# Kernel optimization log

Hardware: AMD Instinct MI355X
Metric: run time of the kernel (lower is better)

Reference implementation:

```python
import jax, jax.numpy as jnp
import numpy as np

D_MODEL = 1024
N_HEADS = 16
D_K = D_MODEL // N_HEADS
SCALE = float(np.sqrt(D_K))


def setup_inputs() -> dict:
    key = jax.random.key(0)
    ks = jax.random.split(key, 6)
    B, S = 2, 2048
    lim_qkv = 1.0 / np.sqrt(D_MODEL)
    x = jax.random.normal(ks[0], (B, S, D_MODEL), dtype=jnp.float32)
    mask = jnp.ones((B, S), dtype=jnp.int32)
    W_qkv = jax.random.uniform(ks[1], (D_MODEL, 3 * D_MODEL), jnp.float32, -lim_qkv, lim_qkv)
    b_qkv = jax.random.uniform(ks[2], (3 * D_MODEL,), jnp.float32, -lim_qkv, lim_qkv)
    W_out = jax.random.uniform(ks[3], (D_MODEL, D_MODEL), jnp.float32, -lim_qkv, lim_qkv)
    b_out = jax.random.uniform(ks[4], (D_MODEL,), jnp.float32, -lim_qkv, lim_qkv)
    return {"x": x, "mask": mask, "W_qkv": W_qkv, "b_qkv": b_qkv, "W_out": W_out, "b_out": b_out}


def reference(x, mask, W_qkv, b_qkv, W_out, b_out):
    B, S, _ = x.shape
    qkv = x @ W_qkv + b_qkv                                  # [B,S,3*D]
    qkv = qkv.reshape(B, S, 3, N_HEADS, D_K)
    qkv = jnp.transpose(qkv, (2, 0, 3, 1, 4))                # [3,B,H,S,Dk]
    q, k, v = qkv[0], qkv[1], qkv[2]
    scores = jnp.einsum('bhqd,bhkd->bhqk', q, k) / SCALE      # [B,H,S,S]
    m = mask[:, None, None, :]                               # [B,1,1,S]
    scores = jnp.where(m == 0, jnp.float32(-1e9), scores)
    attn = jax.nn.softmax(scores, axis=-1)
    out = jnp.einsum('bhqk,bhkd->bhqd', attn, v)             # [B,H,S,Dk]
    out = jnp.transpose(out, (0, 2, 1, 3)).reshape(B, S, D_MODEL)
    return out @ W_out + b_out
```

## Files before the change

kernel.cpp:

```cpp
#include <hip/hip_runtime.h>
#include <hip/hip_bf16.h>

typedef __attribute__((ext_vector_type(8))) short short8;
typedef __attribute__((ext_vector_type(4))) short short4v;
typedef __attribute__((ext_vector_type(4))) float f32x4;
typedef __attribute__((ext_vector_type(16))) float f32x16;
typedef __attribute__((ext_vector_type(4))) unsigned uint4v;
typedef __attribute__((ext_vector_type(2))) unsigned uint2v;

static constexpr int BATCH = 2, S = 2048, D = 1024, H = 16, DK = 64;
static constexpr int TOK = BATCH * S;
static constexpr int NQKV = 3 * D;
static constexpr float C2 = 0.125f * 1.44269504088896f;

__device__ inline unsigned short f2bf(float f) {
  unsigned int u = __builtin_bit_cast(unsigned int, f);
  unsigned int r = (u + 0x7fffu + ((u >> 16) & 1u)) >> 16;
  return (unsigned short)r;
}

__device__ inline unsigned cvt_pk_bf16(float lo, float hi) {
  unsigned r;
  asm("v_cvt_pk_bf16_f32 %0, %1, %2" : "=v"(r) : "v"(lo), "v"(hi));
  return r;
}

__device__ inline uint2v permswap(unsigned a, unsigned b) {
  return __builtin_amdgcn_permlane32_swap(a, b, false, false);
}

__device__ inline float fexp2(float x) { return __builtin_amdgcn_exp2f(x); }

__device__ inline void gload_lds16(const void* g, void* l) {
  __builtin_amdgcn_global_load_lds((const __attribute__((address_space(1))) void*)g,
                                   (__attribute__((address_space(3))) void*)l, 16, 0, 0);
}

static constexpr int NB_CVT  = (TOK * D / 4) / 256;
static constexpr int NB_WQKV = (NQKV / 32) * (D / 32);
static constexpr int NB_WOUT = (D / 32) * (D / 32);
static constexpr int NB_MASK = TOK / 256;

__global__ __launch_bounds__(256) void k_prep(const float* __restrict__ x,
                                              unsigned short* __restrict__ x_bf,
                                              const float* __restrict__ W_qkv,
                                              unsigned short* __restrict__ wqkv_t,
                                              const float* __restrict__ W_out,
                                              unsigned short* __restrict__ wout_t,
                                              const int* __restrict__ mask,
                                              float* __restrict__ maskadd,
                                              unsigned char* __restrict__ tileflags) {
  __shared__ float tile[32][33];
  const int bi = blockIdx.x;
  const int tid = threadIdx.x;
  if (bi < NB_CVT) {
    const int i = bi * 256 + tid;
    const float4 v = ((const float4*)x)[i];
    short4v o;
    o[0] = (short)f2bf(v.x); o[1] = (short)f2bf(v.y);
    o[2] = (short)f2bf(v.z); o[3] = (short)f2bf(v.w);
    ((short4v*)x_bf)[i] = o;
    return;
  }
  if (bi < NB_CVT + NB_WQKV + NB_WOUT) {
    const int tbi = bi - NB_CVT;
    const float* in; unsigned short* out; int C, bx, by;
    if (tbi < NB_WQKV) { in = W_qkv; out = wqkv_t; C = NQKV; bx = tbi % (NQKV / 32); by = tbi / (NQKV / 32); }
    else { const int u = tbi - NB_WQKV; in = W_out; out = wout_t; C = D; bx = u % (D / 32); by = u / (D / 32); }
    const int tx = tid & 31, ty = tid >> 5;
    const int bc = bx * 32, br = by * 32;
#pragma unroll
    for (int i = 0; i < 32; i += 8)
      tile[ty + i][tx] = in[(size_t)(br + ty + i) * C + bc + tx];
    __syncthreads();
#pragma unroll
    for (int i = 0; i < 32; i += 8)
      out[(size_t)(bc + ty + i) * D + br + tx] = f2bf(tile[tx][ty + i]);
    return;
  }
  {
    const int j = (bi - NB_CVT - NB_WQKV - NB_WOUT) * 256 + tid;
    const int mv = mask[j];
    maskadd[j] = mv ? 0.f : -1.0e9f;
    const unsigned long long bal = __ballot(mv == 0);
    if ((tid & 63) == 0) tileflags[j >> 6] = (bal != 0ull) ? 1 : 0;
  }
}

template <int QKV_MODE>
__global__ __launch_bounds__(256, 3) void k_gemm(const unsigned short* __restrict__ A,
                                                 const unsigned short* __restrict__ Bt,
                                                 const float* __restrict__ bias,
                                                 void* __restrict__ Cout,
                                                 unsigned short* __restrict__ vt,
                                                 int M, int N, int K) {
  __shared__ alignas(16) unsigned short As[128 * 64];
  __shared__ alignas(16) unsigned short Bs[128 * 64];
  const int tid = threadIdx.x;
  const int wid = tid >> 6, lane = tid & 63;
  const int lr = lane & 15, lg = lane >> 4;
  const int nbx = N >> 7;
  const int bx = blockIdx.x % nbx, by = blockIdx.x / nbx;
  const int m0 = by << 7, n0 = bx << 7;
  const int wm = (wid >> 1) << 6, wn = (wid & 1) << 6;

  f32x4 acc[4][4] = {};

  const int sk = ((lane & 7) ^ (lane >> 3)) << 4;
  const int srow = lane >> 3;

  const int ktc = K >> 6;
  for (int kt = 0; kt < ktc; ++kt) {
    const int k0 = kt << 6;
    __syncthreads();
#pragma unroll
    for (int c = 0; c < 4; ++c) {
      const int chunk = c * 4 + wid;
      const int mrow = chunk * 8 + srow;
      const char* ga = (const char*)(A + (size_t)(m0 + mrow) * K + k0) + sk;
      gload_lds16(ga, (char*)As + chunk * 1024);
      const char* gb = (const char*)(Bt + (size_t)(n0 + mrow) * K + k0) + sk;
      gload_lds16(gb, (char*)Bs + chunk * 1024);
    }
    __syncthreads();
#pragma unroll
    for (int ks = 0; ks < 2; ++ks) {
      const int kb = ks * 64 + lg * 16;
      const int swz = (lr & 7) << 4;
      short8 af[4], bfr[4];
#pragma unroll
      for (int mf = 0; mf < 4; ++mf) {
        const int m = wm + mf * 16 + lr;
        af[mf] = *(const short8*)((const char*)As + m * 128 + (kb ^ swz));
      }
#pragma unroll
      for (int nf = 0; nf < 4; ++nf) {
        const int n = wn + nf * 16 + lr;
        bfr[nf] = *(const short8*)((const char*)Bs + n * 128 + (kb ^ swz));
      }
#pragma unroll
      for (int mf = 0; mf < 4; ++mf)
#pragma unroll
        for (int nf = 0; nf < 4; ++nf)
          acc[mf][nf] = __builtin_amdgcn_mfma_f32_16x16x32_bf16(af[mf], bfr[nf], acc[mf][nf], 0, 0, 0);
    }
  }
#pragma unroll
  for (int nf = 0; nf < 4; ++nf) {
    const int n = n0 + wn + nf * 16 + lr;
    const float bv = bias[n];
    if (QKV_MODE) {
      if (n < 2 * D) {
        const float scl = (n < D) ? C2 : 1.0f;
#pragma unroll
        for (int mf = 0; mf < 4; ++mf)
#pragma unroll
          for (int r = 0; r < 4; ++r) {
            const int m = m0 + wm + mf * 16 + lg * 4 + r;
            ((unsigned short*)Cout)[(size_t)m * N + n] = f2bf((acc[mf][nf][r] + bv) * scl);
          }
      } else {
        const int dd = n - 2 * D;
        const int hh = dd >> 6, dk = dd & 63;
#pragma unroll
        for (int mf = 0; mf < 4; ++mf) {
          const int mbase = m0 + wm + mf * 16 + lg * 4;
          const int bb = mbase >> 11;
          const int ss = mbase & (S - 1);
          uint2 w;
          w.x = cvt_pk_bf16(acc[mf][nf][0] + bv, acc[mf][nf][1] + bv);
          w.y = cvt_pk_bf16(acc[mf][nf][2] + bv, acc[mf][nf][3] + bv);
          *(uint2*)(vt + ((size_t)((bb * H + hh) * DK + dk)) * S + ss) = w;
        }
      }
    } else {
#pragma unroll
      for (int mf = 0; mf < 4; ++mf)
#pragma unroll
        for (int r = 0; r < 4; ++r) {
          const int m = m0 + wm + mf * 16 + lg * 4 + r;
          ((float*)Cout)[(size_t)m * N + n] = acc[mf][nf][r] + bv;
        }
    }
  }
}

__global__ __launch_bounds__(256, 2) void k_attn(const unsigned short* __restrict__ qkv,
                                                 const unsigned short* __restrict__ vt,
                                                 const float* __restrict__ maskadd,
                                                 const unsigned char* __restrict__ tileflags,
                                                 unsigned short* __restrict__ attn) {
  __shared__ alignas(16) char Ks[2][16384];
  __shared__ alignas(16) char Vs[2][16384];

  constexpr int NT = S / 128;

  const int blk = blockIdx.x;
  const int work = (blk & 7) * 64 + (blk >> 3);
  const int qt = work & 15;
  const int bh = work >> 4;
  const int b = bh >> 4, h = bh & 15;
  const int tid = threadIdx.x;
  const int wid = tid >> 6, lane = tid & 63;
  const int l5 = lane & 31, hw = lane >> 5;
  const int q0 = qt * 128 + wid * 32;
  const int q = q0 + l5;

  const unsigned char* bflags = tileflags + b * (S / 64);

  const unsigned short* qrow = qkv + (size_t)(b * S + q) * NQKV + h * DK;
  short8 qf[4];
#pragma unroll
  for (int ks = 0; ks < 4; ++ks)
    qf[ks] = *(const short8*)(qrow + ks * 16 + hw * 8);

  const unsigned short* kg0 = qkv + ((size_t)b * S * NQKV + D + h * DK);
  const unsigned short* vg0 = vt + (size_t)bh * DK * S;
  const int srow8 = lane >> 3;
  const int skk = ((lane & 7) ^ srow8) << 4;
  const int vrow4 = lane >> 4;

  auto stage = [&](int buf, int kt) {
    const int kbase = kt * 128;
#pragma unroll
    for (int i = 0; i < 4; ++i) {
      const int ck = wid + i * 4;
      const int krow = ck * 8 + srow8;
      gload_lds16((const char*)(kg0 + (size_t)(kbase + krow) * NQKV) + skk,
                  Ks[buf] + ck * 1024);
      const int cv = wid + i * 4;
      const int vr = cv * 4 + vrow4;
      const int ss = (lane & 15) ^ (vr & 15);
      gload_lds16((const char*)(vg0 + (size_t)vr * S + kbase + ss * 8),
                  Vs[buf] + cv * 1024);
    }
  };

  f32x16 o[2] = {};
  float lpart = 0.f;

  const int rswz8 = (l5 & 7) << 4;
  const int rswz16 = (l5 & 15) << 4;

  stage(0, 0);

  int cur = 0;
  for (int kt = 0; kt < NT; ++kt) {
    asm volatile("s_waitcnt vmcnt(0)" ::: "memory");
    __builtin_amdgcn_s_barrier();
    __builtin_amdgcn_sched_barrier(0);
    if (kt + 1 < NT) stage(cur ^ 1, kt + 1);

    const int kbase = kt * 128;

    f32x16 sc[4];
    __builtin_amdgcn_s_setprio(1);
#pragma unroll
    for (int kh = 0; kh < 4; ++kh) {
      f32x16 t2 = {};
#pragma unroll
      for (int ks = 0; ks < 4; ++ks) {
        const short8 kf = *(const short8*)(Ks[cur] + (kh * 32 + l5) * 128 +
                                           ((ks * 32 + hw * 16) ^ rswz8));
        t2 = __builtin_amdgcn_mfma_f32_32x32x16_bf16(kf, qf[ks], t2, 0, 0, 0);
      }
      sc[kh] = t2;
    }
    __builtin_amdgcn_s_setprio(0);

    short8 vf[2][8];
#pragma unroll
    for (int dh = 0; dh < 2; ++dh)
#pragma unroll
      for (int s = 0; s < 8; ++s)
        vf[dh][s] = *(const short8*)(Vs[cur] + (dh * 32 + l5) * 256 +
                                     ((s * 32 + hw * 16) ^ rswz16));

    if (bflags[2 * kt] | bflags[2 * kt + 1]) {
#pragma unroll
      for (int kh = 0; kh < 4; ++kh)
#pragma unroll
        for (int m = 0; m < 4; ++m) {
          const f32x4 a4 = *(const f32x4*)(maskadd + b * S + kbase + kh * 32 + m * 8 + hw * 4);
#pragma unroll
          for (int r = 0; r < 4; ++r)
            sc[kh][m * 4 + r] += a4[r];
        }
    }

    float ps = 0.f;
#pragma unroll
    for (int kh = 0; kh < 4; ++kh) {
#pragma unroll
      for (int r = 0; r < 16; ++r)
        sc[kh][r] = fexp2(sc[kh][r]);
#pragma unroll
      for (int m = 0; m < 4; ++m)
        ps += (sc[kh][4 * m] + sc[kh][4 * m + 1]) + (sc[kh][4 * m + 2] + sc[kh][4 * m + 3]);

      const unsigned c00 = cvt_pk_bf16(sc[kh][0], sc[kh][1]);
      const unsigned c01 = cvt_pk_bf16(sc[kh][2], sc[kh][3]);
      const unsigned c10 = cvt_pk_bf16(sc[kh][4], sc[kh][5]);
      const unsigned c11 = cvt_pk_bf16(sc[kh][6], sc[kh][7]);
      const unsigned c20 = cvt_pk_bf16(sc[kh][8], sc[kh][9]);
      const unsigned c21 = cvt_pk_bf16(sc[kh][10], sc[kh][11]);
      const unsigned c30 = cvt_pk_bf16(sc[kh][12], sc[kh][13]);
      const unsigned c31 = cvt_pk_bf16(sc[kh][14], sc[kh][15]);
      const uint2v r0 = permswap(c00, c10);
      const uint2v r1 = permswap(c01, c11);
      const uint2v r2 = permswap(c20, c30);
      const uint2v r3 = permswap(c21, c31);
      uint4v p0, p1;
      p0[0] = r0[0]; p0[2] = r0[1]; p0[1] = r1[0]; p0[3] = r1[1];
      p1[0] = r2[0]; p1[2] = r2[1]; p1[1] = r3[0]; p1[3] = r3[1];
      const short8 pb0 = __builtin_bit_cast(short8, p0);
      const short8 pb1 = __builtin_bit_cast(short8, p1);

      __builtin_amdgcn_s_setprio(1);
#pragma unroll
      for (int dh = 0; dh < 2; ++dh) {
        o[dh] = __builtin_amdgcn_mfma_f32_32x32x16_bf16(vf[dh][2 * kh], pb0, o[dh], 0, 0, 0);
        o[dh] = __builtin_amdgcn_mfma_f32_32x32x16_bf16(vf[dh][2 * kh + 1], pb1, o[dh], 0, 0, 0);
      }
      __builtin_amdgcn_s_setprio(0);
    }
    lpart += ps;

    cur ^= 1;
  }

  const float ls = lpart + __shfl_xor(lpart, 32);
  const float inv = 1.0f / ls;
  unsigned short* orow = attn + (size_t)(b * S + q) * D + h * DK;
#pragma unroll
  for (int dh = 0; dh < 2; ++dh)
#pragma unroll
    for (int m = 0; m < 4; ++m) {
      const int d = dh * 32 + m * 8 + hw * 4;
      uint2 w;
      w.x = cvt_pk_bf16(o[dh][4 * m + 0] * inv, o[dh][4 * m + 1] * inv);
      w.y = cvt_pk_bf16(o[dh][4 * m + 2] * inv, o[dh][4 * m + 3] * inv);
      *(uint2*)(orow + d) = w;
    }
}

extern "C" void kernel_launch(void* const* d_in, const int* in_sizes, int n_in,
                              void* d_out, int out_size, void* d_ws, size_t ws_size,
                              hipStream_t stream) {
  const float* x = (const float*)d_in[0];
  const int* mask = (const int*)d_in[1];
  const float* W_qkv = (const float*)d_in[2];
  const float* b_qkv = (const float*)d_in[3];
  const float* W_out = (const float*)d_in[4];
  const float* b_out = (const float*)d_in[5];
  float* out = (float*)d_out;

  char* ws = (char*)d_ws;
  unsigned short* x_bf   = (unsigned short*)(ws);
  unsigned short* wqkv_t = (unsigned short*)(ws + (size_t)(8 << 20));
  unsigned short* wout_t = (unsigned short*)(ws + (size_t)(14 << 20));
  unsigned short* qkv    = (unsigned short*)(ws + (size_t)(16 << 20));
  unsigned short* vtr    = (unsigned short*)(ws + (size_t)(40 << 20));
  unsigned short* attn   = (unsigned short*)(ws + (size_t)(48 << 20));
  float*          madd   = (float*)(ws + (size_t)(56 << 20));
  unsigned char*  tflags = (unsigned char*)(ws + (size_t)(56 << 20) + 16384);

  k_prep<<<NB_CVT + NB_WQKV + NB_WOUT + NB_MASK, 256, 0, stream>>>(
      x, x_bf, W_qkv, wqkv_t, W_out, wout_t, mask, madd, tflags);
  k_gemm<1><<<(TOK / 128) * (NQKV / 128), 256, 0, stream>>>(x_bf, wqkv_t, b_qkv, qkv, vtr, TOK, NQKV, D);
  k_attn<<<BATCH * H * (S / 128), 256, 0, stream>>>(qkv, vtr, madd, tflags, attn);
  k_gemm<0><<<(TOK / 128) * (D / 128), 256, 0, stream>>>(attn, wout_t, b_out, out, nullptr, TOK, D, D);
}
```

Measured before the change: 105.6 us.

## Split attention key range into two halves with a separate combine kernel

```diff
diff --git a/kernel.cpp b/kernel.cpp
--- a/kernel.cpp
+++ b/kernel.cpp
@@ -11,12 +11,17 @@
 static constexpr int BATCH = 2, S = 2048, D = 1024, H = 16, DK = 64;
 static constexpr int TOK = BATCH * S;
 static constexpr int NQKV = 3 * D;
+static constexpr int NBH = BATCH * H;
 static constexpr float C2 = 0.125f * 1.44269504088896f;
 
 __device__ inline unsigned short f2bf(float f) {
   unsigned int u = __builtin_bit_cast(unsigned int, f);
   unsigned int r = (u + 0x7fffu + ((u >> 16) & 1u)) >> 16;
   return (unsigned short)r;
+}
+
+__device__ inline float bf2f(unsigned short u) {
+  return __builtin_bit_cast(float, (unsigned)u << 16);
 }
 
 __device__ inline unsigned cvt_pk_bf16(float lo, float hi) {
@@ -185,26 +190,31 @@
   }
 }
 
-__global__ __launch_bounds__(256, 2) void k_attn(const unsigned short* __restrict__ qkv,
+__global__ __launch_bounds__(512, 4) void k_attn(const unsigned short* __restrict__ qkv,
                                                  const unsigned short* __restrict__ vt,
                                                  const float* __restrict__ maskadd,
                                                  const unsigned char* __restrict__ tileflags,
-                                                 unsigned short* __restrict__ attn) {
+                                                 unsigned short* __restrict__ po0,
+                                                 unsigned short* __restrict__ po1,
+                                                 float* __restrict__ lbuf) {
   __shared__ alignas(16) char Ks[2][16384];
   __shared__ alignas(16) char Vs[2][16384];
 
-  constexpr int NT = S / 128;
+  constexpr int NTH = 8;
 
   const int blk = blockIdx.x;
   const int work = (blk & 7) * 64 + (blk >> 3);
-  const int qt = work & 15;
   const int bh = work >> 4;
+  const int rem = work & 15;
+  const int qt = rem >> 1;
+  const int half = rem & 1;
   const int b = bh >> 4, h = bh & 15;
   const int tid = threadIdx.x;
   const int wid = tid >> 6, lane = tid & 63;
   const int l5 = lane & 31, hw = lane >> 5;
-  const int q0 = qt * 128 + wid * 32;
+  const int q0 = qt * 256 + wid * 32;
   const int q = q0 + l5;
+  const int kt0 = half * NTH;
 
   const unsigned char* bflags = tileflags + b * (S / 64);
 
@@ -223,12 +233,12 @@
   auto stage = [&](int buf, int kt) {
     const int kbase = kt * 128;
 #pragma unroll
-    for (int i = 0; i < 4; ++i) {
-      const int ck = wid + i * 4;
+    for (int i = 0; i < 2; ++i) {
+      const int ck = wid + i * 8;
       const int krow = ck * 8 + srow8;
       gload_lds16((const char*)(kg0 + (size_t)(kbase + krow) * NQKV) + skk,
                   Ks[buf] + ck * 1024);
-      const int cv = wid + i * 4;
+      const int cv = wid + i * 8;
       const int vr = cv * 4 + vrow4;
       const int ss = (lane & 15) ^ (vr & 15);
       gload_lds16((const char*)(vg0 + (size_t)vr * S + kbase + ss * 8),
@@ -242,14 +252,15 @@
   const int rswz8 = (l5 & 7) << 4;
   const int rswz16 = (l5 & 15) << 4;
 
-  stage(0, 0);
+  stage(0, kt0);
 
   int cur = 0;
-  for (int kt = 0; kt < NT; ++kt) {
+  for (int t = 0; t < NTH; ++t) {
+    const int kt = kt0 + t;
     asm volatile("s_waitcnt vmcnt(0)" ::: "memory");
     __builtin_amdgcn_s_barrier();
     __builtin_amdgcn_sched_barrier(0);
-    if (kt + 1 < NT) stage(cur ^ 1, kt + 1);
+    if (t + 1 < NTH) stage(cur ^ 1, kt + 1);
 
     const int kbase = kt * 128;
 
@@ -330,18 +341,48 @@
   }
 
   const float ls = lpart + __shfl_xor(lpart, 32);
-  const float inv = 1.0f / ls;
+  unsigned short* po = (half ? po1 : po0) + ((size_t)bh * S + q) * DK;
+#pragma unroll
+  for (int dh = 0; dh < 2; ++dh)
+#pragma unroll
+    for (int m = 0; m < 4; ++m) {
+      uint2 w;
+      w.x = cvt_pk_bf16(o[dh][4 * m + 0], o[dh][4 * m + 1]);
+      w.y = cvt_pk_bf16(o[dh][4 * m + 2], o[dh][4 * m + 3]);
+      *(uint2*)(po + dh * 32 + m * 8 + hw * 4) = w;
+    }
+  if (hw == 0) lbuf[((size_t)(half * NBH + bh)) * S + q] = ls;
+}
+
+__global__ __launch_bounds__(256) void k_combine(const unsigned short* __restrict__ po0,
+                                                 const unsigned short* __restrict__ po1,
+                                                 const float* __restrict__ lbuf,
+                                                 unsigned short* __restrict__ attn) {
+  const int bh = blockIdx.x >> 3;
+  const int q = ((blockIdx.x & 7) << 8) + threadIdx.x;
+  const int b = bh >> 4, h = bh & 15;
+
+  const float l0 = lbuf[(size_t)bh * S + q];
+  const float l1 = lbuf[((size_t)(NBH + bh)) * S + q];
+  const float inv = 1.0f / (l0 + l1);
+
+  const unsigned short* r0 = po0 + ((size_t)bh * S + q) * DK;
+  const unsigned short* r1 = po1 + ((size_t)bh * S + q) * DK;
   unsigned short* orow = attn + (size_t)(b * S + q) * D + h * DK;
 #pragma unroll
-  for (int dh = 0; dh < 2; ++dh)
-#pragma unroll
-    for (int m = 0; m < 4; ++m) {
-      const int d = dh * 32 + m * 8 + hw * 4;
-      uint2 w;
-      w.x = cvt_pk_bf16(o[dh][4 * m + 0] * inv, o[dh][4 * m + 1] * inv);
-      w.y = cvt_pk_bf16(o[dh][4 * m + 2] * inv, o[dh][4 * m + 3] * inv);
-      *(uint2*)(orow + d) = w;
-    }
+  for (int c = 0; c < 8; ++c) {
+    const short8 a = *(const short8*)(r0 + c * 8);
+    const short8 bb = *(const short8*)(r1 + c * 8);
+    unsigned wv[4];
+#pragma unroll
+    for (int p = 0; p < 4; ++p) {
+      const float v0 = (bf2f((unsigned short)a[2 * p]) + bf2f((unsigned short)bb[2 * p])) * inv;
+      const float v1 = (bf2f((unsigned short)a[2 * p + 1]) + bf2f((unsigned short)bb[2 * p + 1])) * inv;
+      wv[p] = cvt_pk_bf16(v0, v1);
+    }
+    uint4v u; u[0] = wv[0]; u[1] = wv[1]; u[2] = wv[2]; u[3] = wv[3];
+    *(uint4v*)(orow + c * 8) = u;
+  }
 }
 
 extern "C" void kernel_launch(void* const* d_in, const int* in_sizes, int n_in,
@@ -361,13 +402,17 @@
   unsigned short* wout_t = (unsigned short*)(ws + (size_t)(14 << 20));
   unsigned short* qkv    = (unsigned short*)(ws + (size_t)(16 << 20));
   unsigned short* vtr    = (unsigned short*)(ws + (size_t)(40 << 20));
-  unsigned short* attn   = (unsigned short*)(ws + (size_t)(48 << 20));
   float*          madd   = (float*)(ws + (size_t)(56 << 20));
   unsigned char*  tflags = (unsigned char*)(ws + (size_t)(56 << 20) + 16384);
+  float*          lbuf   = (float*)(ws + (size_t)(56 << 20) + 65536);
+  unsigned short* po0    = x_bf;
+  unsigned short* po1    = (unsigned short*)(ws + (size_t)(48 << 20));
+  unsigned short* attn   = qkv;
 
   k_prep<<<NB_CVT + NB_WQKV + NB_WOUT + NB_MASK, 256, 0, stream>>>(
       x, x_bf, W_qkv, wqkv_t, W_out, wout_t, mask, madd, tflags);
   k_gemm<1><<<(TOK / 128) * (NQKV / 128), 256, 0, stream>>>(x_bf, wqkv_t, b_qkv, qkv, vtr, TOK, NQKV, D);
-  k_attn<<<BATCH * H * (S / 128), 256, 0, stream>>>(qkv, vtr, madd, tflags, attn);
+  k_attn<<<BATCH * H * (S / 256) * 2, 512, 0, stream>>>(qkv, vtr, madd, tflags, po0, po1, lbuf);
+  k_combine<<<NBH * (S / 256), 256, 0, stream>>>(po0, po1, lbuf, attn);
   k_gemm<0><<<(TOK / 128) * (D / 128), 256, 0, stream>>>(attn, wout_t, b_out, out, nullptr, TOK, D, D);
 }
```

New measurement: 255.4 us. +141.9%, slower.
